# Kernel tuning notes

Measured on AMD Instinct MI355X. Metric: run time of the kernel, lower is better.

## Reference

```python
import jax, jax.numpy as jnp
import numpy as np

B, L, C = 2, 2048, 1024
H, HD = 16, 64
MAX_SCALE_MUL = float(np.log(100.0))
SCALE = 1.0  # attn_l2_norm=True -> scale is 1


def setup_inputs() -> dict:
    key = jax.random.key(0)
    ks = jax.random.split(key, 6)
    x = jax.random.normal(ks[0], (B, L, C), dtype=jnp.float32)
    attn_bias = jax.random.normal(ks[1], (1, 1, L, L), dtype=jnp.float32)
    w_qkv = jax.random.normal(ks[2], (3 * C, C), dtype=jnp.float32) * (1.0 / np.sqrt(C))
    q_bias = jnp.zeros((C,), dtype=jnp.float32)
    v_bias = jnp.zeros((C,), dtype=jnp.float32)
    scale_mul = jnp.full((1, H, 1, 1), np.log(4.0), dtype=jnp.float32)  # scale_mul_1H11
    w_proj = jax.random.normal(ks[3], (C, C), dtype=jnp.float32) * (1.0 / np.sqrt(C))
    b_proj = jnp.zeros((C,), dtype=jnp.float32)
    return {"x": x, "attn_bias": attn_bias, "w_qkv": w_qkv, "q_bias": q_bias,
            "v_bias": v_bias, "scale_mul": scale_mul, "w_proj": w_proj, "b_proj": b_proj}


def reference(x, attn_bias, w_qkv, q_bias, v_bias, scale_mul, w_proj, b_proj):
    # qkv projection with concatenated bias (q_bias, zeros, v_bias)
    bias = jnp.concatenate([q_bias, jnp.zeros_like(q_bias), v_bias])  # [3C]
    qkv = jnp.einsum('blc,dc->bld', x, w_qkv) + bias                  # [B,L,3C]
    qkv = qkv.reshape(B, L, 3, H, HD).transpose(2, 0, 3, 1, 4)        # [3,B,H,L,HD]
    q, k, v = qkv[0], qkv[1], qkv[2]
    # attn_l2_norm path: L2-normalize q,k; q scaled by exp(clamped scale_mul)
    sm = jnp.exp(jnp.minimum(scale_mul, MAX_SCALE_MUL))               # [1,H,1,1]
    q = q / jnp.linalg.norm(q, axis=-1, keepdims=True) * sm
    k = k / jnp.linalg.norm(k, axis=-1, keepdims=True)
    # slow_attn: scaled scores + bias, softmax, weighted sum
    attn = jnp.einsum('bhld,bhmd->bhlm', q * SCALE, k) + attn_bias    # [B,H,L,L]
    p = jax.nn.softmax(attn, axis=-1)
    oup = jnp.einsum('bhlm,bhmd->bhld', p, v)                         # [B,H,L,HD]
    oup = oup.transpose(0, 2, 1, 3).reshape(B, L, C)
    return jnp.einsum('blc,dc->bld', oup, w_proj) + b_proj
```

## Files before the change

### kernel.cpp

```cpp
#include <hip/hip_runtime.h>
#include <cstdint>
#include <cstddef>
#include <math.h>

typedef __attribute__((ext_vector_type(8))) __bf16 bf16x8;
typedef __attribute__((ext_vector_type(4))) __bf16 bf16x4;
typedef __attribute__((ext_vector_type(4))) float f32x4;
typedef __attribute__((ext_vector_type(4))) unsigned int u32x4;

#define AS1 __attribute__((address_space(1)))
#define AS3 __attribute__((address_space(3)))

#define LOG2E 1.4426950408889634f

__device__ __forceinline__ void gld16(void* lds_uniform, const void* gaddr) {
  __builtin_amdgcn_global_load_lds((const AS1 unsigned int*)gaddr,
                                   (AS3 unsigned int*)lds_uniform, 16, 0, 0);
}

__global__ __launch_bounds__(256)
void prep_kernel(const float* __restrict__ x, const float* __restrict__ wqkv,
                 const float* __restrict__ wproj, const float* __restrict__ bias,
                 __bf16* __restrict__ xb, __bf16* __restrict__ wqkvb,
                 __bf16* __restrict__ wprojb, __bf16* __restrict__ btr) {
  __shared__ __bf16 T[32][264];
  const int b = blockIdx.x;
  const int tid = threadIdx.x;
  if (b < 8192) {
    const float* src; __bf16* dst; int off;
    if (b < 4096)      { src = x;     dst = xb;     off = b; }
    else if (b < 7168) { src = wqkv;  dst = wqkvb;  off = b - 4096; }
    else               { src = wproj; dst = wprojb; off = b - 7168; }
    const int i = (off * 256 + tid) * 4;
    const float4 v = *(const float4*)(src + i);
    bf16x4 o;
    o[0] = (__bf16)v.x; o[1] = (__bf16)v.y; o[2] = (__bf16)v.z; o[3] = (__bf16)v.w;
    *(bf16x4*)(dst + i) = o;
    return;
  }
  const int bb = b - 8192;
  const int rb = bb >> 3, cg = bb & 7;
  const float* src = bias + (size_t)(rb * 32) * 2048 + cg * 256;
#pragma unroll
  for (int i = 0; i < 8; ++i) {
    const int u = i * 256 + tid;
    const int r = u >> 6, c4 = (u & 63) * 4;
    const float4 v = *(const float4*)(src + (size_t)r * 2048 + c4);
    T[r][c4 + 0] = (__bf16)(v.x * LOG2E);
    T[r][c4 + 1] = (__bf16)(v.y * LOG2E);
    T[r][c4 + 2] = (__bf16)(v.z * LOG2E);
    T[r][c4 + 3] = (__bf16)(v.w * LOG2E);
  }
  __syncthreads();
  const int ktl = tid >> 6;
  const int lane = tid & 63, g = lane >> 4, cc = lane & 15;
#pragma unroll
  for (int sub = 0; sub < 2; ++sub) {
    __bf16 outv[16];
#pragma unroll
    for (int v = 0; v < 16; ++v) {
      const int ni = v >> 2, j = v & 3;
      outv[v] = T[sub * 16 + cc][ktl * 64 + ni * 16 + g * 4 + j];
    }
    __bf16* dst = btr + ((size_t)(((rb * 2 + sub) * 32) + cg * 4 + ktl) * 64 + lane) * 16;
    *(bf16x8*)(dst) = *(bf16x8*)(outv);
    *(bf16x8*)(dst + 8) = *(bf16x8*)(outv + 8);
  }
}

__global__ __launch_bounds__(256, 2)
void gemm_qkv_kernel(const __bf16* __restrict__ A, const __bf16* __restrict__ B,
                     const float* __restrict__ q_bias, const float* __restrict__ v_bias,
                     const float* __restrict__ scale_mul,
                     __bf16* __restrict__ qb, __bf16* __restrict__ ktp, __bf16* __restrict__ vb) {
  __shared__ __attribute__((aligned(16))) __bf16 As[128 * 32];
  __shared__ __attribute__((aligned(16))) __bf16 Bs[128 * 32];
  const int tid = threadIdx.x;
  const int w = tid >> 6, lane = tid & 63;
  const int m0 = blockIdx.y * 128, n0 = blockIdx.x * 128;
  const int wm = (w >> 1) * 64, wn = (w & 1) * 64;
  const int c = lane & 15, g = lane >> 4;
  f32x4 acc[4][4];
#pragma unroll
  for (int i = 0; i < 4; ++i)
#pragma unroll
    for (int j = 0; j < 4; ++j) acc[i][j] = (f32x4)(0.0f);

  const int r_row = lane >> 2;
  const int r_col = (lane & 3) * 16;
  const char* Abase = (const char*)A + (size_t)m0 * 2048;
  const char* Bbase = (const char*)B + (size_t)n0 * 2048;

  for (int kt = 0; kt < 1024; kt += 32) {
#pragma unroll
    for (int s = 0; s < 2; ++s) {
      const int R = w * 2 + s;
      const int row = R * 16 + r_row;
      gld16((char*)As + R * 1024, Abase + (size_t)row * 2048 + kt * 2 + r_col);
      gld16((char*)Bs + R * 1024, Bbase + (size_t)row * 2048 + kt * 2 + r_col);
    }
    __syncthreads();
    bf16x8 af[4], bfr[4];
#pragma unroll
    for (int i = 0; i < 4; ++i) {
      af[i]  = *(const bf16x8*)((const char*)As + (wm + i * 16 + c) * 64 + g * 16);
      bfr[i] = *(const bf16x8*)((const char*)Bs + (wn + i * 16 + c) * 64 + g * 16);
    }
#pragma unroll
    for (int ni = 0; ni < 4; ++ni)
#pragma unroll
      for (int mi = 0; mi < 4; ++mi)
        acc[ni][mi] = __builtin_amdgcn_mfma_f32_16x16x32_bf16(bfr[ni], af[mi], acc[ni][mi], 0, 0, 0);
    __syncthreads();
  }

  const int nbase = n0 + wn;
  const int which = nbase >> 10;
  const int h = (nbase >> 6) & 15;
  float smh = 1.0f;
  if (which == 0) smh = __expf(fminf(scale_mul[h], 4.605170185988091f)) * LOG2E;
  float4 cb[4];
#pragma unroll
  for (int ni = 0; ni < 4; ++ni) {
    if (which == 0)      cb[ni] = *(const float4*)(q_bias + nbase + ni * 16 + 4 * g);
    else if (which == 2) cb[ni] = *(const float4*)(v_bias + nbase - 2048 + ni * 16 + 4 * g);
    else                 cb[ni] = make_float4(0.f, 0.f, 0.f, 0.f);
  }
  const int mrow0 = m0 + wm;
  const int b2 = mrow0 >> 11;
  const int lpos0 = mrow0 & 2047;
  __bf16* kt_tile = ktp + (size_t)(b2 * 16 + h) * 131072 + (size_t)(lpos0 >> 6) * 4096;
  __bf16* dst_qv = ((which == 0) ? qb : vb) + ((size_t)((b2 * 16 + h) * 2048 + lpos0)) * 64;

#pragma unroll
  for (int mi = 0; mi < 4; ++mi) {
    float v[4][4];
    float ss = 0.0f;
#pragma unroll
    for (int ni = 0; ni < 4; ++ni) {
      v[ni][0] = acc[ni][mi][0] + cb[ni].x;
      v[ni][1] = acc[ni][mi][1] + cb[ni].y;
      v[ni][2] = acc[ni][mi][2] + cb[ni].z;
      v[ni][3] = acc[ni][mi][3] + cb[ni].w;
#pragma unroll
      for (int j = 0; j < 4; ++j) ss += v[ni][j] * v[ni][j];
    }
    ss += __shfl_xor(ss, 16, 64);
    ss += __shfl_xor(ss, 32, 64);
    const float sc = (which == 2) ? 1.0f : (rsqrtf(ss) * smh);
    const int key = mi * 16 + c;
    if (which == 1) {
#pragma unroll
      for (int ni = 0; ni < 4; ++ni) {
        bf16x4 pk;
        pk[0] = (__bf16)(v[ni][0] * sc); pk[1] = (__bf16)(v[ni][1] * sc);
        pk[2] = (__bf16)(v[ni][2] * sc); pk[3] = (__bf16)(v[ni][3] * sc);
        *(bf16x4*)(kt_tile + (ni >> 1) * 2048 + key * 32 + (ni & 1) * 16 + 4 * g) = pk;
      }
    } else {
      __bf16* drow = dst_qv + (size_t)key * 64;
#pragma unroll
      for (int ni = 0; ni < 4; ++ni) {
        bf16x4 pk;
        pk[0] = (__bf16)(v[ni][0] * sc); pk[1] = (__bf16)(v[ni][1] * sc);
        pk[2] = (__bf16)(v[ni][2] * sc); pk[3] = (__bf16)(v[ni][3] * sc);
        *(bf16x4*)(drow + ni * 16 + 4 * g) = pk;
      }
    }
  }
}

__global__ __launch_bounds__(256)
void vtrans_kernel(const __bf16* __restrict__ vb, __bf16* __restrict__ vtp) {
  __shared__ __attribute__((aligned(16))) __bf16 Vs[4][64 * 64];
  const int w = threadIdx.x >> 6, lane = threadIdx.x & 63;
  const int idx = blockIdx.x * 4 + w;
  const int bh = idx >> 5, tile = idx & 31;
  const __bf16* src = vb + ((size_t)bh * 2048 + tile * 64) * 64;
#pragma unroll
  for (int s = 0; s < 8; ++s)
    gld16((char*)&Vs[w][0] + s * 1024, (const char*)src + s * 1024 + lane * 16);
  __syncthreads();
  __bf16* outb = vtp + (size_t)idx * 4096;
  const int gg = lane & 3, cc = lane >> 2;
#pragma unroll
  for (int r = 0; r < 8; ++r) {
    const int o = r * 512 + lane * 8;
    const int ni = r & 3, ks = r >> 2;
    const int hd = ni * 16 + cc;
    const int key0 = ks * 32 + gg * 8;
    bf16x8 pk;
#pragma unroll
    for (int i = 0; i < 8; ++i)
      pk[i] = Vs[w][(key0 + i) * 64 + hd];
    *(bf16x8*)(outb + o) = pk;
  }
}

#define STAGE(t, b) {                                                          \
  const char* _ks = kp + (size_t)(t) * 8192 + w * 1024 + sl16;                 \
  const char* _vs = vp + (size_t)(t) * 8192 + w * 1024 + sl16;                 \
  gld16(&Kb[b][w * 1024], _ks);                                                \
  gld16(&Vb[b][w * 1024], _vs);                                                \
}

#define BAV(ni, j) ((ni * 4 + j < 8) ? bA0[(ni * 4 + j) & 7] : bA1[(ni * 4 + j) & 7])

#define COMPUTE(t, b) {                                                        \
  const char* _bb = bp + (size_t)(t) * 2048 + lane * 32;                       \
  bf16x8 bA0 = *(const bf16x8*)_bb;                                            \
  bf16x8 bA1 = *(const bf16x8*)(_bb + 16);                                     \
  bf16x8 kf[4][2];                                                             \
  _Pragma("unroll")                                                            \
  for (int ni = 0; ni < 4; ++ni)                                               \
    _Pragma("unroll")                                                          \
    for (int ks = 0; ks < 2; ++ks)                                             \
      kf[ni][ks] = *(const bf16x8*)(&Kb[b][0] + ks * 4096 + (ni * 16 + c) * 64 + gsw16); \
  f32x4 sacc[4];                                                               \
  __builtin_amdgcn_s_setprio(1);                                               \
  _Pragma("unroll")                                                            \
  for (int ni = 0; ni < 4; ++ni) {                                             \
    f32x4 s_ = __builtin_amdgcn_mfma_f32_16x16x32_bf16(kf[ni][0], qf[0], (f32x4)(0.0f), 0, 0, 0); \
    sacc[ni] = __builtin_amdgcn_mfma_f32_16x16x32_bf16(kf[ni][1], qf[1], s_, 0, 0, 0); \
  }                                                                            \
  __builtin_amdgcn_s_setprio(0);                                               \
  unsigned qp[4][2];                                                           \
  _Pragma("unroll")                                                            \
  for (int ni = 0; ni < 4; ++ni) {                                             \
    const float p0 = __builtin_amdgcn_exp2f(sacc[ni][0] + (float)BAV(ni, 0));  \
    const float p1 = __builtin_amdgcn_exp2f(sacc[ni][1] + (float)BAV(ni, 1));  \
    const float p2 = __builtin_amdgcn_exp2f(sacc[ni][2] + (float)BAV(ni, 2));  \
    const float p3 = __builtin_amdgcn_exp2f(sacc[ni][3] + (float)BAV(ni, 3));  \
    lsum += (p0 + p1) + (p2 + p3);                                             \
    asm("v_cvt_pk_bf16_f32 %0, %1, %2" : "=v"(qp[ni][0]) : "v"(p0), "v"(p1));  \
    asm("v_cvt_pk_bf16_f32 %0, %1, %2" : "=v"(qp[ni][1]) : "v"(p2), "v"(p3));  \
  }                                                                            \
  bf16x8 pf[2];                                                                \
  _Pragma("unroll")                                                            \
  for (int ks = 0; ks < 2; ++ks) {                                             \
    unsigned x0 = qp[2 * ks][0], x1 = qp[2 * ks][1];                           \
    unsigned y0 = qp[2 * ks + 1][0], y1 = qp[2 * ks + 1][1];                   \
    asm("v_permlane32_swap_b32 %0, %1" : "+v"(x0), "+v"(y0));                  \
    asm("v_permlane16_swap_b32 %0, %1" : "+v"(x0), "+v"(y0));                  \
    asm("v_permlane32_swap_b32 %0, %1" : "+v"(x1), "+v"(y1));                  \
    asm("v_permlane16_swap_b32 %0, %1" : "+v"(x1), "+v"(y1));                  \
    u32x4 t_; t_[0] = x0; t_[1] = x1; t_[2] = y0; t_[3] = y1;                  \
    pf[ks] = __builtin_bit_cast(bf16x8, t_);                                   \
  }                                                                            \
  __builtin_amdgcn_s_setprio(1);                                               \
  _Pragma("unroll")                                                            \
  for (int ni = 0; ni < 4; ++ni) {                                             \
    const bf16x8 v0 = *(const bf16x8*)(&Vb[b][0] + 0 * 4096 + ni * 1024 + c * 64 + gsw16); \
    const bf16x8 v1 = *(const bf16x8*)(&Vb[b][0] + 1 * 4096 + ni * 1024 + c * 64 + gsw16); \
    oacc[ni] = __builtin_amdgcn_mfma_f32_16x16x32_bf16(pf[0], v0, oacc[ni], 0, 0, 0); \
    oacc[ni] = __builtin_amdgcn_mfma_f32_16x16x32_bf16(pf[1], v1, oacc[ni], 0, 0, 0); \
  }                                                                            \
  __builtin_amdgcn_s_setprio(0);                                               \
}

__global__ __launch_bounds__(512, 4)
void attn_kernel(const __bf16* __restrict__ qb, const __bf16* __restrict__ ktp,
                 const __bf16* __restrict__ vtp, const __bf16* __restrict__ btr,
                 __bf16* __restrict__ oupb) {
  __shared__ __attribute__((aligned(16))) char Kb[2][8192];
  __shared__ __attribute__((aligned(16))) char Vb[2][8192];
  const int tid = threadIdx.x, w = tid >> 6, lane = tid & 63;
  const int c = lane & 15, g = lane >> 4;
  const int sl16 = (lane ^ ((lane >> 3) & 3)) * 16;
  const int gsw16 = (g ^ ((c >> 1) & 3)) * 16;
  const int idx = blockIdx.x;
  const int bh = idx & 31, rb = idx >> 5;
  const __bf16* qh = qb + (size_t)bh * (2048 * 64);
  const char* kp = (const char*)ktp + (size_t)bh * (32 * 8192);
  const char* vp = (const char*)vtp + (size_t)bh * (32 * 8192);
  const char* bp = (const char*)btr + (size_t)(rb * 8 + w) * 65536;
  const int q0 = rb * 128 + w * 16;
  const int b2 = bh >> 4, h = bh & 15;

  bf16x8 qf[2];
#pragma unroll
  for (int ks = 0; ks < 2; ++ks)
    qf[ks] = *(const bf16x8*)(qh + (size_t)(q0 + c) * 64 + ks * 32 + g * 8);

  f32x4 oacc[4];
  float lsum = 0.0f;
#pragma unroll
  for (int ni = 0; ni < 4; ++ni) oacc[ni] = (f32x4)(0.0f);

  STAGE(0, 0);
  __syncthreads();
#pragma unroll 1
  for (int tt = 0; tt < 32; tt += 2) {
    if (tt + 1 < 32) STAGE(tt + 1, 1);
    COMPUTE(tt, 0);
    __syncthreads();
    if (tt + 2 < 32) STAGE(tt + 2, 0);
    COMPUTE(tt + 1, 1);
    __syncthreads();
  }

  float l = lsum;
  l += __shfl_xor(l, 16, 64);
  l += __shfl_xor(l, 32, 64);
#pragma unroll
  for (int j = 0; j < 4; ++j) {
    const float lr = __shfl(l, g * 4 + j, 64);
    const float inv = 1.0f / lr;
    const int qrow = q0 + g * 4 + j;
    __bf16* orow = oupb + ((size_t)(b2 * 2048 + qrow) * 16 + h) * 64;
#pragma unroll
    for (int ni = 0; ni < 4; ++ni)
      orow[ni * 16 + c] = (__bf16)(oacc[ni][j] * inv);
  }
}

__global__ __launch_bounds__(256, 2)
void gemm_proj_kernel(const __bf16* __restrict__ A, const __bf16* __restrict__ B,
                      const float* __restrict__ b_proj, float* __restrict__ out) {
  __shared__ __attribute__((aligned(16))) __bf16 As[64 * 32];
  __shared__ __attribute__((aligned(16))) __bf16 Bs[128 * 32];
  const int tid = threadIdx.x;
  const int w = tid >> 6, lane = tid & 63;
  const int c = lane & 15, g = lane >> 4;
  const int m0 = blockIdx.y * 64, n0 = blockIdx.x * 128;
  const int wm = (w >> 1) * 32, wn = (w & 1) * 64;
  f32x4 acc[2][4];
#pragma unroll
  for (int i = 0; i < 2; ++i)
#pragma unroll
    for (int j = 0; j < 4; ++j) acc[i][j] = (f32x4)(0.0f);

  const int r_row = lane >> 2;
  const int r_col = (lane & 3) * 16;
  const char* Abase = (const char*)A + (size_t)m0 * 2048;
  const char* Bbase = (const char*)B + (size_t)n0 * 2048;

  for (int kt = 0; kt < 1024; kt += 32) {
    {
      const int row = w * 16 + r_row;
      gld16((char*)As + w * 1024, Abase + (size_t)row * 2048 + kt * 2 + r_col);
    }
#pragma unroll
    for (int s = 0; s < 2; ++s) {
      const int R = w * 2 + s;
      const int row = R * 16 + r_row;
      gld16((char*)Bs + R * 1024, Bbase + (size_t)row * 2048 + kt * 2 + r_col);
    }
    __syncthreads();
    bf16x8 af[2], bfr[4];
#pragma unroll
    for (int i = 0; i < 2; ++i)
      af[i] = *(const bf16x8*)((const char*)As + (wm + i * 16 + c) * 64 + g * 16);
#pragma unroll
    for (int i = 0; i < 4; ++i)
      bfr[i] = *(const bf16x8*)((const char*)Bs + (wn + i * 16 + c) * 64 + g * 16);
#pragma unroll
    for (int mi = 0; mi < 2; ++mi)
#pragma unroll
      for (int ni = 0; ni < 4; ++ni)
        acc[mi][ni] = __builtin_amdgcn_mfma_f32_16x16x32_bf16(af[mi], bfr[ni], acc[mi][ni], 0, 0, 0);
    __syncthreads();
  }

  float cbias[4];
#pragma unroll
  for (int ni = 0; ni < 4; ++ni) cbias[ni] = b_proj[n0 + wn + ni * 16 + c];
#pragma unroll
  for (int mi = 0; mi < 2; ++mi)
#pragma unroll
    for (int j = 0; j < 4; ++j) {
      const int m = m0 + wm + mi * 16 + g * 4 + j;
      float* orow = out + (size_t)m * 1024 + n0 + wn;
#pragma unroll
      for (int ni = 0; ni < 4; ++ni)
        orow[ni * 16 + c] = acc[mi][ni][j] + cbias[ni];
    }
}

extern "C" void kernel_launch(void* const* d_in, const int* in_sizes, int n_in,
                              void* d_out, int out_size, void* d_ws, size_t ws_size,
                              hipStream_t stream) {
  const float* x         = (const float*)d_in[0];
  const float* attn_bias = (const float*)d_in[1];
  const float* w_qkv     = (const float*)d_in[2];
  const float* q_bias    = (const float*)d_in[3];
  const float* v_bias    = (const float*)d_in[4];
  const float* scale_mul = (const float*)d_in[5];
  const float* w_proj    = (const float*)d_in[6];
  const float* b_proj    = (const float*)d_in[7];
  float* out = (float*)d_out;

  __bf16* xb     = (__bf16*)d_ws;
  __bf16* wqkvb  = xb + 4194304;
  __bf16* wprojb = wqkvb + 3145728;
  __bf16* qb     = wprojb + 1048576;
  __bf16* ktp    = qb + 4194304;
  __bf16* vtp    = ktp + 4194304;
  __bf16* btr    = vtp + 4194304;
  __bf16* vb     = btr + 4194304;
  __bf16* oupb   = xb;

  prep_kernel<<<8704, 256, 0, stream>>>(x, w_qkv, w_proj, attn_bias, xb, wqkvb, wprojb, btr);
  gemm_qkv_kernel<<<dim3(24, 32), 256, 0, stream>>>(xb, wqkvb, q_bias, v_bias, scale_mul,
                                                    qb, ktp, vb);
  vtrans_kernel<<<256, 256, 0, stream>>>(vb, vtp);
  attn_kernel<<<512, 512, 0, stream>>>(qb, ktp, vtp, btr, oupb);
  gemm_proj_kernel<<<dim3(8, 64), 256, 0, stream>>>(oupb, wprojb, b_proj, out);
}
```

Baseline: 216.2 us.

## Process two query tiles per wave to reuse K/V fragments in attention

The attention kernel now runs 4 waves per block, not 8, and each wave handles 32 query rows as two 16-row m-tiles. K fragments and V loads from LDS are reused across both tiles, and each wave stages twice as much K/V per tile. This halves LDS reads of K/V per query row and lets the second tile's QK MFMAs interleave with the first tile's softmax. It raises register pressure and leaves fewer waves per block to hide latency.

```diff
diff --git a/kernel.cpp b/kernel.cpp
--- a/kernel.cpp
+++ b/kernel.cpp
@@ -198,44 +198,28 @@
 }
 
 #define STAGE(t, b) {                                                          \
-  const char* _ks = kp + (size_t)(t) * 8192 + w * 1024 + sl16;                 \
-  const char* _vs = vp + (size_t)(t) * 8192 + w * 1024 + sl16;                 \
-  gld16(&Kb[b][w * 1024], _ks);                                                \
-  gld16(&Vb[b][w * 1024], _vs);                                                \
-}
-
-#define BAV(ni, j) ((ni * 4 + j < 8) ? bA0[(ni * 4 + j) & 7] : bA1[(ni * 4 + j) & 7])
-
-#define COMPUTE(t, b) {                                                        \
-  const char* _bb = bp + (size_t)(t) * 2048 + lane * 32;                       \
-  bf16x8 bA0 = *(const bf16x8*)_bb;                                            \
-  bf16x8 bA1 = *(const bf16x8*)(_bb + 16);                                     \
-  bf16x8 kf[4][2];                                                             \
-  _Pragma("unroll")                                                            \
-  for (int ni = 0; ni < 4; ++ni)                                               \
-    _Pragma("unroll")                                                          \
-    for (int ks = 0; ks < 2; ++ks)                                             \
-      kf[ni][ks] = *(const bf16x8*)(&Kb[b][0] + ks * 4096 + (ni * 16 + c) * 64 + gsw16); \
-  f32x4 sacc[4];                                                               \
-  __builtin_amdgcn_s_setprio(1);                                               \
+  const char* _ks = kp + (size_t)(t) * 8192 + w * 2048;                        \
+  const char* _vs = vp + (size_t)(t) * 8192 + w * 2048;                        \
+  gld16(&Kb[b][w * 2048],        _ks + sl16);                                  \
+  gld16(&Kb[b][w * 2048 + 1024], _ks + 1024 + sl16);                           \
+  gld16(&Vb[b][w * 2048],        _vs + sl16);                                  \
+  gld16(&Vb[b][w * 2048 + 1024], _vs + 1024 + sl16);                           \
+}
+
+#define BAV(ba0, ba1, ni, j) ((ni * 4 + j < 8) ? ba0[(ni * 4 + j) & 7] : ba1[(ni * 4 + j) & 7])
+
+#define SOFTMAX(sacc, ba0, ba1, pf, ls) {                                      \
+  unsigned qp[4][2];                                                           \
   _Pragma("unroll")                                                            \
   for (int ni = 0; ni < 4; ++ni) {                                             \
-    f32x4 s_ = __builtin_amdgcn_mfma_f32_16x16x32_bf16(kf[ni][0], qf[0], (f32x4)(0.0f), 0, 0, 0); \
-    sacc[ni] = __builtin_amdgcn_mfma_f32_16x16x32_bf16(kf[ni][1], qf[1], s_, 0, 0, 0); \
-  }                                                                            \
-  __builtin_amdgcn_s_setprio(0);                                               \
-  unsigned qp[4][2];                                                           \
-  _Pragma("unroll")                                                            \
-  for (int ni = 0; ni < 4; ++ni) {                                             \
-    const float p0 = __builtin_amdgcn_exp2f(sacc[ni][0] + (float)BAV(ni, 0));  \
-    const float p1 = __builtin_amdgcn_exp2f(sacc[ni][1] + (float)BAV(ni, 1));  \
-    const float p2 = __builtin_amdgcn_exp2f(sacc[ni][2] + (float)BAV(ni, 2));  \
-    const float p3 = __builtin_amdgcn_exp2f(sacc[ni][3] + (float)BAV(ni, 3));  \
-    lsum += (p0 + p1) + (p2 + p3);                                             \
+    const float p0 = __builtin_amdgcn_exp2f(sacc[ni][0] + (float)BAV(ba0, ba1, ni, 0)); \
+    const float p1 = __builtin_amdgcn_exp2f(sacc[ni][1] + (float)BAV(ba0, ba1, ni, 1)); \
+    const float p2 = __builtin_amdgcn_exp2f(sacc[ni][2] + (float)BAV(ba0, ba1, ni, 2)); \
+    const float p3 = __builtin_amdgcn_exp2f(sacc[ni][3] + (float)BAV(ba0, ba1, ni, 3)); \
+    ls += (p0 + p1) + (p2 + p3);                                               \
     asm("v_cvt_pk_bf16_f32 %0, %1, %2" : "=v"(qp[ni][0]) : "v"(p0), "v"(p1));  \
     asm("v_cvt_pk_bf16_f32 %0, %1, %2" : "=v"(qp[ni][1]) : "v"(p2), "v"(p3));  \
   }                                                                            \
-  bf16x8 pf[2];                                                                \
   _Pragma("unroll")                                                            \
   for (int ks = 0; ks < 2; ++ks) {                                             \
     unsigned x0 = qp[2 * ks][0], x1 = qp[2 * ks][1];                           \
@@ -247,18 +231,55 @@
     u32x4 t_; t_[0] = x0; t_[1] = x1; t_[2] = y0; t_[3] = y1;                  \
     pf[ks] = __builtin_bit_cast(bf16x8, t_);                                   \
   }                                                                            \
+}
+
+#define COMPUTE(t, b) {                                                        \
+  const char* _ba = bpA + (size_t)(t) * 2048 + lane * 32;                      \
+  bf16x8 bA0 = *(const bf16x8*)_ba;                                            \
+  bf16x8 bA1 = *(const bf16x8*)(_ba + 16);                                     \
+  bf16x8 kf[4][2];                                                             \
+  _Pragma("unroll")                                                            \
+  for (int ni = 0; ni < 4; ++ni)                                               \
+    _Pragma("unroll")                                                          \
+    for (int ks = 0; ks < 2; ++ks)                                             \
+      kf[ni][ks] = *(const bf16x8*)(&Kb[b][0] + ks * 4096 + (ni * 16 + c) * 64 + gsw16); \
+  f32x4 sacc[4];                                                               \
+  __builtin_amdgcn_s_setprio(1);                                               \
+  _Pragma("unroll")                                                            \
+  for (int ni = 0; ni < 4; ++ni) {                                             \
+    f32x4 s_ = __builtin_amdgcn_mfma_f32_16x16x32_bf16(kf[ni][0], qf[0][0], (f32x4)(0.0f), 0, 0, 0); \
+    sacc[ni] = __builtin_amdgcn_mfma_f32_16x16x32_bf16(kf[ni][1], qf[0][1], s_, 0, 0, 0); \
+  }                                                                            \
+  __builtin_amdgcn_s_setprio(0);                                               \
+  const char* _bb2 = bpB + (size_t)(t) * 2048 + lane * 32;                     \
+  bf16x8 bB0 = *(const bf16x8*)_bb2;                                           \
+  bf16x8 bB1 = *(const bf16x8*)(_bb2 + 16);                                    \
+  bf16x8 pf0[2];                                                               \
+  SOFTMAX(sacc, bA0, bA1, pf0, lsum[0]);                                       \
+  f32x4 sacc2[4];                                                              \
+  __builtin_amdgcn_s_setprio(1);                                               \
+  _Pragma("unroll")                                                            \
+  for (int ni = 0; ni < 4; ++ni) {                                             \
+    f32x4 s_ = __builtin_amdgcn_mfma_f32_16x16x32_bf16(kf[ni][0], qf[1][0], (f32x4)(0.0f), 0, 0, 0); \
+    sacc2[ni] = __builtin_amdgcn_mfma_f32_16x16x32_bf16(kf[ni][1], qf[1][1], s_, 0, 0, 0); \
+  }                                                                            \
+  __builtin_amdgcn_s_setprio(0);                                               \
+  bf16x8 pf1[2];                                                               \
+  SOFTMAX(sacc2, bB0, bB1, pf1, lsum[1]);                                      \
   __builtin_amdgcn_s_setprio(1);                                               \
   _Pragma("unroll")                                                            \
   for (int ni = 0; ni < 4; ++ni) {                                             \
     const bf16x8 v0 = *(const bf16x8*)(&Vb[b][0] + 0 * 4096 + ni * 1024 + c * 64 + gsw16); \
     const bf16x8 v1 = *(const bf16x8*)(&Vb[b][0] + 1 * 4096 + ni * 1024 + c * 64 + gsw16); \
-    oacc[ni] = __builtin_amdgcn_mfma_f32_16x16x32_bf16(pf[0], v0, oacc[ni], 0, 0, 0); \
-    oacc[ni] = __builtin_amdgcn_mfma_f32_16x16x32_bf16(pf[1], v1, oacc[ni], 0, 0, 0); \
+    oacc[0][ni] = __builtin_amdgcn_mfma_f32_16x16x32_bf16(pf0[0], v0, oacc[0][ni], 0, 0, 0); \
+    oacc[0][ni] = __builtin_amdgcn_mfma_f32_16x16x32_bf16(pf0[1], v1, oacc[0][ni], 0, 0, 0); \
+    oacc[1][ni] = __builtin_amdgcn_mfma_f32_16x16x32_bf16(pf1[0], v0, oacc[1][ni], 0, 0, 0); \
+    oacc[1][ni] = __builtin_amdgcn_mfma_f32_16x16x32_bf16(pf1[1], v1, oacc[1][ni], 0, 0, 0); \
   }                                                                            \
   __builtin_amdgcn_s_setprio(0);                                               \
 }
 
-__global__ __launch_bounds__(512, 4)
+__global__ __launch_bounds__(256, 4)
 void attn_kernel(const __bf16* __restrict__ qb, const __bf16* __restrict__ ktp,
                  const __bf16* __restrict__ vtp, const __bf16* __restrict__ btr,
                  __bf16* __restrict__ oupb) {
@@ -273,19 +294,26 @@
   const __bf16* qh = qb + (size_t)bh * (2048 * 64);
   const char* kp = (const char*)ktp + (size_t)bh * (32 * 8192);
   const char* vp = (const char*)vtp + (size_t)bh * (32 * 8192);
-  const char* bp = (const char*)btr + (size_t)(rb * 8 + w) * 65536;
-  const int q0 = rb * 128 + w * 16;
+  const char* bpA = (const char*)btr + (size_t)(rb * 8 + w * 2) * 65536;
+  const char* bpB = bpA + 65536;
+  const int q0 = rb * 128 + w * 32;
   const int b2 = bh >> 4, h = bh & 15;
 
-  bf16x8 qf[2];
-#pragma unroll
-  for (int ks = 0; ks < 2; ++ks)
-    qf[ks] = *(const bf16x8*)(qh + (size_t)(q0 + c) * 64 + ks * 32 + g * 8);
-
-  f32x4 oacc[4];
-  float lsum = 0.0f;
-#pragma unroll
-  for (int ni = 0; ni < 4; ++ni) oacc[ni] = (f32x4)(0.0f);
+  bf16x8 qf[2][2];
+#pragma unroll
+  for (int mi = 0; mi < 2; ++mi)
+#pragma unroll
+    for (int ks = 0; ks < 2; ++ks)
+      qf[mi][ks] = *(const bf16x8*)(qh + (size_t)(q0 + mi * 16 + c) * 64 + ks * 32 + g * 8);
+
+  f32x4 oacc[2][4];
+  float lsum[2];
+#pragma unroll
+  for (int mi = 0; mi < 2; ++mi) {
+    lsum[mi] = 0.0f;
+#pragma unroll
+    for (int ni = 0; ni < 4; ++ni) oacc[mi][ni] = (f32x4)(0.0f);
+  }
 
   STAGE(0, 0);
   __syncthreads();
@@ -299,18 +327,21 @@
     __syncthreads();
   }
 
-  float l = lsum;
-  l += __shfl_xor(l, 16, 64);
-  l += __shfl_xor(l, 32, 64);
-#pragma unroll
-  for (int j = 0; j < 4; ++j) {
-    const float lr = __shfl(l, g * 4 + j, 64);
-    const float inv = 1.0f / lr;
-    const int qrow = q0 + g * 4 + j;
-    __bf16* orow = oupb + ((size_t)(b2 * 2048 + qrow) * 16 + h) * 64;
-#pragma unroll
-    for (int ni = 0; ni < 4; ++ni)
-      orow[ni * 16 + c] = (__bf16)(oacc[ni][j] * inv);
+#pragma unroll
+  for (int mi = 0; mi < 2; ++mi) {
+    float l = lsum[mi];
+    l += __shfl_xor(l, 16, 64);
+    l += __shfl_xor(l, 32, 64);
+#pragma unroll
+    for (int j = 0; j < 4; ++j) {
+      const float lr = __shfl(l, g * 4 + j, 64);
+      const float inv = 1.0f / lr;
+      const int qrow = q0 + mi * 16 + g * 4 + j;
+      __bf16* orow = oupb + ((size_t)(b2 * 2048 + qrow) * 16 + h) * 64;
+#pragma unroll
+      for (int ni = 0; ni < 4; ++ni)
+        orow[ni * 16 + c] = (__bf16)(oacc[mi][ni][j] * inv);
+    }
   }
 }
 
@@ -404,6 +435,6 @@
   gemm_qkv_kernel<<<dim3(24, 32), 256, 0, stream>>>(xb, wqkvb, q_bias, v_bias, scale_mul,
                                                     qb, ktp, vb);
   vtrans_kernel<<<256, 256, 0, stream>>>(vb, vtp);
-  attn_kernel<<<512, 512, 0, stream>>>(qb, ktp, vtp, btr, oupb);
+  attn_kernel<<<512, 256, 0, stream>>>(qb, ktp, vtp, btr, oupb);
   gemm_proj_kernel<<<dim3(8, 64), 256, 0, stream>>>(oupb, wprojb, b_proj, out);
 }
```

Result: slower. 239.4 us (+10.7%).

## Triple-buffer K/V tiles in attention with explicit vmcnt waits and single barrier

Applied to the files above, without the earlier changes.

Moves the attention kernel's K/V staging from a double buffer to a triple buffer that prefetches two tiles ahead. The two __syncthreads per tile pair become one s_barrier per tile, guarded by a manual `s_waitcnt vmcnt(2)`, and the per-tile bias loads are hoisted to the top of each iteration ahead of the stage issue. The goal is to hide more global-load latency and cut barrier overhead. In exchange, LDS per block grows to 48KB, which may lower resident blocks per CU. The hand-written vmcnt counts must also stay exact near the end of the loop, where no new stage is issued.

```diff
diff --git a/kernel.cpp b/kernel.cpp
--- a/kernel.cpp
+++ b/kernel.cpp
@@ -197,7 +197,7 @@
   }
 }
 
-#define STAGE(t, b) {                                                          \
+#define STAGE3(t, b) {                                                         \
   const char* _ks = kp + (size_t)(t) * 8192 + w * 1024 + sl16;                 \
   const char* _vs = vp + (size_t)(t) * 8192 + w * 1024 + sl16;                 \
   gld16(&Kb[b][w * 1024], _ks);                                                \
@@ -206,10 +206,7 @@
 
 #define BAV(ni, j) ((ni * 4 + j < 8) ? bA0[(ni * 4 + j) & 7] : bA1[(ni * 4 + j) & 7])
 
-#define COMPUTE(t, b) {                                                        \
-  const char* _bb = bp + (size_t)(t) * 2048 + lane * 32;                       \
-  bf16x8 bA0 = *(const bf16x8*)_bb;                                            \
-  bf16x8 bA1 = *(const bf16x8*)(_bb + 16);                                     \
+#define COMPUTE3(b) {                                                          \
   bf16x8 kf[4][2];                                                             \
   _Pragma("unroll")                                                            \
   for (int ni = 0; ni < 4; ++ni)                                               \
@@ -262,8 +259,8 @@
 void attn_kernel(const __bf16* __restrict__ qb, const __bf16* __restrict__ ktp,
                  const __bf16* __restrict__ vtp, const __bf16* __restrict__ btr,
                  __bf16* __restrict__ oupb) {
-  __shared__ __attribute__((aligned(16))) char Kb[2][8192];
-  __shared__ __attribute__((aligned(16))) char Vb[2][8192];
+  __shared__ __attribute__((aligned(16))) char Kb[3][8192];
+  __shared__ __attribute__((aligned(16))) char Vb[3][8192];
   const int tid = threadIdx.x, w = tid >> 6, lane = tid & 63;
   const int c = lane & 15, g = lane >> 4;
   const int sl16 = (lane ^ ((lane >> 3) & 3)) * 16;
@@ -287,16 +284,29 @@
 #pragma unroll
   for (int ni = 0; ni < 4; ++ni) oacc[ni] = (f32x4)(0.0f);
 
-  STAGE(0, 0);
-  __syncthreads();
+  STAGE3(0, 0);
+  STAGE3(1, 1);
+  asm volatile("s_waitcnt vmcnt(2)" ::: "memory");
+  __builtin_amdgcn_sched_barrier(0);
+  __builtin_amdgcn_s_barrier();
+
+  int bsel = 0;
 #pragma unroll 1
-  for (int tt = 0; tt < 32; tt += 2) {
-    if (tt + 1 < 32) STAGE(tt + 1, 1);
-    COMPUTE(tt, 0);
-    __syncthreads();
-    if (tt + 2 < 32) STAGE(tt + 2, 0);
-    COMPUTE(tt + 1, 1);
-    __syncthreads();
+  for (int tt = 0; tt < 32; ++tt) {
+    const char* _bb = bp + (size_t)tt * 2048 + lane * 32;
+    bf16x8 bA0 = *(const bf16x8*)_bb;
+    bf16x8 bA1 = *(const bf16x8*)(_bb + 16);
+    __builtin_amdgcn_sched_barrier(0);
+    if (tt < 30) {
+      const int bn = (bsel + 2 >= 3) ? (bsel - 1) : (bsel + 2);
+      STAGE3(tt + 2, bn);
+    }
+    __builtin_amdgcn_sched_barrier(0);
+    COMPUTE3(bsel);
+    asm volatile("s_waitcnt vmcnt(2)" ::: "memory");
+    __builtin_amdgcn_sched_barrier(0);
+    __builtin_amdgcn_s_barrier();
+    bsel = (bsel + 1 == 3) ? 0 : (bsel + 1);
   }
 
   float l = lsum;
```

New measurement: 220.3 us. No clear change (+1.9%).
